# Performance work log

Measured on AMD Instinct MI355X. Metric: run time of the kernel, lower is better.

The kernel has to match this reference:

```python
import jax, jax.numpy as jnp
import numpy as np

B, C, D, H = 128, 8, 1024, 8
K_RANGE = (2, 3, 4, 5)


def setup_inputs() -> dict:
    key = jax.random.key(0)
    ks = jax.random.split(key, 10)
    s = 0.02
    return {
        "x": jax.random.normal(ks[0], (B, D), jnp.float32),
        # per-K prototype groups, shape (nb_classes, K, embed_dim) as in get_prototype_group()
        "p2": jax.random.normal(ks[1], (C, 2, D), jnp.float32),
        "p3": jax.random.normal(ks[2], (C, 3, D), jnp.float32),
        "p4": jax.random.normal(ks[3], (C, 4, D), jnp.float32),
        "p5": jax.random.normal(ks[4], (C, 5, D), jnp.float32),
        # per-class attention Block params (stacked over class axis)
        "ln_g": jnp.ones((C, D), jnp.float32),
        "ln_b": jnp.zeros((C, D), jnp.float32),
        "w_qkv": jax.random.normal(ks[5], (C, 3 * D, D), jnp.float32) * s,
        "b_qkv": jnp.zeros((C, 3 * D), jnp.float32),
        "w_proj": jax.random.normal(ks[6], (C, D, D), jnp.float32) * s,
        "b_proj": jnp.zeros((C, D), jnp.float32),
        # cls head
        "w_cls": jax.random.normal(ks[7], (C, D), jnp.float32) * s,
        "b_cls": jnp.zeros((C,), jnp.float32),
    }


def _proto_group(x, pg):
    """x: (B,D); pg: (C,K,D). Returns nearest proto (B,D), per-sample class group (B,K,D), class ids (B,)."""
    Cc, K, d = pg.shape
    flat = pg.reshape(Cc * K, d)
    # squared L2 distances (argmin identical to torch.cdist p=2 argmin)
    d2 = (jnp.sum(x * x, axis=1, keepdims=True)
          - 2.0 * (x @ flat.T)
          + jnp.sum(flat * flat, axis=1))
    idx = jnp.argmin(d2, axis=1)          # (B,)
    cls = idx // K                        # (B,)
    return flat[idx], pg[cls], cls


def _vicreg(x, nearest, proto_space, sim_c=25.0, std_c=25.0, cov_c=1.0):
    # sim: pull x toward its nearest prototype in every K-group
    repr_loss = jnp.mean((x[:, None, :] - nearest) ** 2)
    # std over batch of prototype space, unbiased var, eps=1e-4
    std = jnp.sqrt(jnp.var(proto_space, axis=0, ddof=1) + 1e-4)   # (S,D)
    std_loss = jnp.mean(jax.nn.relu(1.0 - std))
    # covariance of centered flattened prototype space
    ps = proto_space - jnp.mean(proto_space, axis=0)
    P = ps.reshape(-1, ps.shape[-1])                              # (B*S, D)
    cov = P.T @ P / (P.shape[0] - 1)
    cov_loss = ((cov ** 2).sum() - (jnp.diagonal(cov) ** 2).sum()) / ps.shape[-1]
    return sim_c * repr_loss + std_c * std_loss + cov_c * cov_loss


def _forward(x, p2, p3, p4, p5, ln_g, ln_b, w_qkv, b_qkv, w_proj, b_proj, w_cls, b_cls):
    groups = (p2, p3, p4, p5)
    nearest_list, space_list, cls = [], [], None
    for pg in groups:
        n, sp, cls = _proto_group(x, pg)   # cls kept from LAST group, as in torch code
        nearest_list.append(n)
        space_list.append(sp)
    nearest = jnp.stack(nearest_list, axis=1)     # (B, len(K_range), D)
    proto_space = jnp.concatenate(space_list, 1)  # (B, sum(K_range), D)

    vcr = _vicreg(x, nearest, proto_space)

    # per-class attention Block: LayerNorm -> MHA -> residual, vectorized over class axis c
    S = proto_space.shape[1]
    mu = proto_space.mean(-1, keepdims=True)
    var = proto_space.var(-1, keepdims=True)
    xn = (proto_space - mu) * jax.lax.rsqrt(var + 1e-5)               # (B,S,D)
    h = xn[None] * ln_g[:, None, None, :] + ln_b[:, None, None, :]    # (C,B,S,D)

    qkv = jnp.einsum('cbsd,cfd->cbsf', h, w_qkv) + b_qkv[:, None, None, :]
    dh = D // H
    qkv = qkv.reshape(C, B, S, 3, H, dh).transpose(3, 0, 1, 4, 2, 5)  # (3,C,B,H,S,dh)
    q, k, v = qkv[0] * (dh ** -0.5), qkv[1], qkv[2]
    attn = jax.nn.softmax(jnp.einsum('cbhqe,cbhke->cbhqk', q, k), axis=-1)
    o = jnp.einsum('cbhqk,cbhke->cbhqe', attn, v)                     # (C,B,H,S,dh)
    o = o.transpose(0, 1, 3, 2, 4).reshape(C, B, S, D)
    out = jnp.einsum('cbsd,ced->cbse', o, w_proj) + b_proj[:, None, None, :]
    attended = proto_space[None] + out                                # (C,B,S,D)

    # route each sample through the block of its (last-group) assigned class
    cond = attended[cls, jnp.arange(B)]                               # (B,S,D)
    cond = cond / jnp.maximum(jnp.linalg.norm(cond, axis=2, keepdims=True), 1e-12)
    pooled = cond.mean(1)                                             # (B,D)
    logits = pooled @ w_cls.T + b_cls
    return logits, vcr


def reference(x, p2, p3, p4, p5, ln_g, ln_b, w_qkv, b_qkv, w_proj, b_proj, w_cls, b_cls):
    return _forward(x, p2, p3, p4, p5, ln_g, ln_b, w_qkv, b_qkv, w_proj, b_proj, w_cls, b_cls)
```

## Files before the change

kernel.cpp:

```cpp
#include <hip/hip_runtime.h>
#include <math.h>

#define NB 128
#define ND 1024
#define NS 14
#define NDH 128

typedef float f32x4 __attribute__((ext_vector_type(4)));
typedef short bf16x8 __attribute__((ext_vector_type(8)));
typedef unsigned int u32x4 __attribute__((ext_vector_type(4)));

__device__ __forceinline__ unsigned short f2bf(float v) {
  unsigned int u = __builtin_bit_cast(unsigned int, v);
  return (unsigned short)((u + 0x7FFFu + ((u >> 16) & 1u)) >> 16);
}
__device__ __forceinline__ float bf2f(unsigned short u) {
  return __builtin_bit_cast(float, (unsigned int)u << 16);
}

__device__ __forceinline__ bf16x8 pack_bv(float4 w0, float4 w1) {
  unsigned int u0, u1, u2, u3;
  asm("v_cvt_pk_bf16_f32 %0, %1, %2" : "=v"(u0) : "v"(w0.x), "v"(w0.y));
  asm("v_cvt_pk_bf16_f32 %0, %1, %2" : "=v"(u1) : "v"(w0.z), "v"(w0.w));
  asm("v_cvt_pk_bf16_f32 %0, %1, %2" : "=v"(u2) : "v"(w1.x), "v"(w1.y));
  asm("v_cvt_pk_bf16_f32 %0, %1, %2" : "=v"(u3) : "v"(w1.z), "v"(w1.w));
  u32x4 u = {u0, u1, u2, u3};
  return __builtin_bit_cast(bf16x8, u);
}

__device__ __forceinline__ void s_decomp(int s, int& g, int& k) {
  if (s < 2)      { g = 0; k = s; }
  else if (s < 5) { g = 1; k = s - 2; }
  else if (s < 9) { g = 2; k = s - 5; }
  else            { g = 3; k = s - 9; }
}
__device__ __forceinline__ const float* grp_ptr(int g, const float* p2, const float* p3,
                                                const float* p4, const float* p5) {
  return g == 0 ? p2 : g == 1 ? p3 : g == 2 ? p4 : p5;
}
__device__ __forceinline__ int grp_base(int g) { return g == 0 ? 0 : g == 1 ? 16 : g == 2 ? 40 : 72; }
__device__ __forceinline__ int grp_k(int g) { return g + 2; }

__global__ __launch_bounds__(256) void k_assign_ln(
    const float* __restrict__ x,
    const float* __restrict__ p2, const float* __restrict__ p3,
    const float* __restrict__ p4, const float* __restrict__ p5,
    const float* __restrict__ ln_g, const float* __restrict__ ln_b,
    unsigned short* __restrict__ hbf2, float* __restrict__ pall,
    int* __restrict__ cls, int* __restrict__ rows_g, float* __restrict__ minv)
{
  int bid = blockIdx.x, t = threadIdx.x;
  __shared__ __align__(16) float xs[ND];
  float4* xs4 = (float4*)xs;
  if (bid < 112) {
    int r = bid;
    const float* pp; int idx;
    if (r < 16)      { pp = p2; idx = r; }
    else if (r < 40) { pp = p3; idx = r - 16; }
    else if (r < 72) { pp = p4; idx = r - 40; }
    else             { pp = p5; idx = r - 72; }
    const float4* row4 = (const float4*)(pp + (size_t)idx * ND);
    float4 v = row4[t];
    xs4[t] = v;
    float s1 = v.x + v.y + v.z + v.w;
    float s2 = v.x * v.x + v.y * v.y + v.z * v.z + v.w * v.w;
    __shared__ float ra[256], rb[256];
    ra[t] = s1; rb[t] = s2; __syncthreads();
    for (int o = 128; o > 0; o >>= 1) { if (t < o) { ra[t] += ra[t + o]; rb[t] += rb[t + o]; } __syncthreads(); }
    __shared__ float mu, rstd;
    if (t == 0) {
      float m = ra[0] * (1.f / 1024.f);
      float var = rb[0] * (1.f / 1024.f) - m * m;
      mu = m; rstd = rsqrtf(var + 1e-5f);
    }
    __syncthreads();
    ((float4*)(pall + (size_t)r * ND))[t] = xs4[t];
    float4 xv = xs4[t];
    float nx = (xv.x - mu) * rstd, ny = (xv.y - mu) * rstd,
          nz = (xv.z - mu) * rstd, nw = (xv.w - mu) * rstd;
    int d0 = t * 4;
    int m = r >> 4, rr = r & 15;
    int kblk = d0 >> 5, qq = (d0 >> 3) & 3, e0 = d0 & 7;
    size_t fidx = (size_t)kblk * 3584 + m * 512 + (qq * 16 + rr) * 8 + e0;
#pragma unroll
    for (int c = 0; c < 8; ++c) {
      float4 g = ((const float4*)(ln_g + (size_t)c * ND))[t];
      float4 bb = ((const float4*)(ln_b + (size_t)c * ND))[t];
      ushort4 u;
      u.x = f2bf(nx * g.x + bb.x); u.y = f2bf(ny * g.y + bb.y);
      u.z = f2bf(nz * g.z + bb.z); u.w = f2bf(nw * g.w + bb.w);
      *(ushort4*)&hbf2[(size_t)c * 114688 + fidx] = u;
    }
  } else {
    int b = bid - 112;
    __shared__ float d2s[112];
    __shared__ int cls_s[4];
    const float4* xg4 = (const float4*)(x + (size_t)b * ND);
    xs4[t] = xg4[t];
    __syncthreads();
    if (t < 112) {
      const float* pp; int idx;
      if (t < 16)      { pp = p2; idx = t; }
      else if (t < 40) { pp = p3; idx = t - 16; }
      else if (t < 72) { pp = p4; idx = t - 40; }
      else             { pp = p5; idx = t - 72; }
      const float4* pr4 = (const float4*)(pp + (size_t)idx * ND);
      float acc = 0.f;
#pragma unroll 8
      for (int d = 0; d < 256; ++d) {
        float4 a = xs4[d], p = pr4[d];
        float dx = a.x - p.x, dy = a.y - p.y, dz = a.z - p.z, dw = a.w - p.w;
        acc += dx * dx + dy * dy + dz * dz + dw * dw;
      }
      d2s[t] = acc;
    }
    __syncthreads();
    if (t < 4) {
      int base = grp_base(t), kg = grp_k(t), cnt = 8 * kg;
      float mv = d2s[base]; int mi = 0;
      for (int j = 1; j < cnt; ++j) { float v = d2s[base + j]; if (v < mv) { mv = v; mi = j; } }
      int c = mi / kg;
      cls[b * 4 + t] = c; cls_s[t] = c;
      minv[b * 4 + t] = mv;
    }
    __syncthreads();
    if (t < NS) {
      int g, k; s_decomp(t, g, k);
      rows_g[b * NS + t] = grp_base(g) + cls_s[g] * grp_k(g) + k;
    }
  }
}

__global__ __launch_bounds__(128) void k_prep(
    const int* __restrict__ cls, const float* __restrict__ minv,
    int* __restrict__ counts, int* __restrict__ ccnt, int* __restrict__ order,
    int* __restrict__ posof, int* __restrict__ chunkidx, int* __restrict__ chunk_c,
    int* __restrict__ chunk_lo, int* __restrict__ chunkN, float* __restrict__ scal)
{
  __shared__ int cnt_s[32];
  __shared__ int cc_s[8];
  __shared__ float red[128];
  int t = threadIdx.x;
  if (t < 32) cnt_s[t] = 0;
  if (t < 8) cc_s[t] = 0;
  if (t < 4) scal[t] = 0.f;
  __syncthreads();
  int c3;
#pragma unroll
  for (int g = 0; g < 4; ++g) {
    int c = cls[t * 4 + g];
    atomicAdd(&cnt_s[g * 8 + c], 1);
    if (g == 3) c3 = c;
  }
  int pos = atomicAdd(&cc_s[c3], 1);
  order[c3 * 128 + pos] = t;
  posof[t] = pos;
  red[t] = minv[t * 4 + 0] + minv[t * 4 + 1] + minv[t * 4 + 2] + minv[t * 4 + 3];
  __syncthreads();
  for (int o = 64; o > 0; o >>= 1) { if (t < o) red[t] += red[t + o]; __syncthreads(); }
  if (t == 0) {
    scal[0] = red[0];
    int T = 0;
    for (int c = 0; c < 8; ++c) {
      chunkidx[c] = T;
      int nch = (cc_s[c] + 15) >> 4;
      for (int j = 0; j < nch; ++j) { chunk_c[T] = c; chunk_lo[T] = j * 16; ++T; }
    }
    chunkN[0] = T;
  }
  if (t < 32) counts[t] = cnt_s[t];
  if (t < 8) ccnt[t] = cc_s[t];
}

__global__ __launch_bounds__(256) void k_stats(
    const float* __restrict__ p2, const float* __restrict__ p3,
    const float* __restrict__ p4, const float* __restrict__ p5,
    const int* __restrict__ counts, float* __restrict__ M, float* __restrict__ scal)
{
  int idx = blockIdx.x * 256 + threadIdx.x;
  int s = idx >> 10, d = idx & 1023;
  int g, k; s_decomp(s, g, k);
  const float* pp = grp_ptr(g, p2, p3, p4, p5);
  int kg = grp_k(g);
  float vc[8], nc[8];
  float sum = 0.f, sumsq = 0.f;
#pragma unroll
  for (int c = 0; c < 8; ++c) {
    float v = pp[((size_t)(c * kg + k)) * ND + d];
    float n = (float)counts[g * 8 + c];
    vc[c] = v; nc[c] = n;
    sum += n * v; sumsq += n * v * v;
  }
  float mean = sum * (1.f / 128.f);
  float var = (sumsq - 128.f * mean * mean) * (1.f / 127.f);
  float sd = sqrtf(var + 1e-4f);
#pragma unroll
  for (int c = 0; c < 8; ++c)
    M[((size_t)(s * 8 + c)) * ND + d] = sqrtf(nc[c] * (1.f / 1791.f)) * (vc[c] - mean);
  float part = fmaxf(1.f - sd, 0.f);
  __shared__ float red[256];
  red[threadIdx.x] = part; __syncthreads();
  for (int o = 128; o > 0; o >>= 1) { if (threadIdx.x < o) red[threadIdx.x] += red[threadIdx.x + o]; __syncthreads(); }
  if (threadIdx.x == 0) atomicAdd(&scal[1], red[0]);
}

__global__ __launch_bounds__(128) void k_gramdiag(const float* __restrict__ M, float* __restrict__ scal)
{
  __shared__ __align__(16) float mi[ND];
  __shared__ float red[128];
  int bid = blockIdx.x, t = threadIdx.x;
  if (bid < 112) {
    float4* mi4 = (float4*)mi;
    const float4* src4 = (const float4*)(M + (size_t)bid * ND);
    for (int d = t; d < 256; d += 128) mi4[d] = src4[d];
    __syncthreads();
    float p = 0.f;
    if (t < 112) {
      const float4* mj4 = (const float4*)(M + (size_t)t * ND);
      float acc = 0.f;
#pragma unroll 8
      for (int d = 0; d < 256; ++d) {
        float4 a = mi4[d], b = mj4[d];
        acc += a.x * b.x + a.y * b.y + a.z * b.z + a.w * b.w;
      }
      p = acc * acc;
    }
    red[t] = p; __syncthreads();
    for (int o = 64; o > 0; o >>= 1) { if (t < o) red[t] += red[t + o]; __syncthreads(); }
    if (t == 0) atomicAdd(&scal[2], red[0]);
  } else {
    int d = (bid - 112) * 128 + t;
    float tsum = 0.f;
    for (int r = 0; r < 112; ++r) { float v = M[(size_t)r * ND + d]; tsum += v * v; }
    red[t] = tsum * tsum; __syncthreads();
    for (int o = 64; o > 0; o >>= 1) { if (t < o) red[t] += red[t + o]; __syncthreads(); }
    if (t == 0) atomicAdd(&scal[3], red[0]);
  }
}

__global__ __launch_bounds__(512) void k_qkv_mfma(
    const unsigned short* __restrict__ hbf2, const float* __restrict__ w_qkv,
    const float* __restrict__ b_qkv, unsigned short* __restrict__ qkv_bf)
{
  __shared__ __align__(16) float lred[3 * 2 * 7 * 256];
  int c = blockIdx.y;
  int t = threadIdx.x, lane = t & 63, wid = t >> 6;
  int cg = wid & 1, ks = wid >> 1;
  int r16 = lane & 15, q = lane >> 4;
  int col = blockIdx.x * 32 + cg * 16 + r16;
  const float* Wp = w_qkv + ((size_t)c * 3072 + col) * ND + ks * 256 + q * 8;
  const unsigned short* Hp = hbf2 + (size_t)c * 114688 + (size_t)(ks * 8) * 3584 + lane * 8;
  f32x4 acc[7] = {};
#pragma unroll
  for (int i = 0; i < 8; ++i) {
    float4 w0 = *(const float4*)(Wp + i * 32);
    float4 w1 = *(const float4*)(Wp + i * 32 + 4);
    bf16x8 bv = pack_bv(w0, w1);
    const unsigned short* hk = Hp + (size_t)i * 3584;
#pragma unroll
    for (int m = 0; m < 7; ++m) {
      bf16x8 av = *(const bf16x8*)(hk + m * 512);
      acc[m] = __builtin_amdgcn_mfma_f32_16x16x32_bf16(av, bv, acc[m], 0, 0, 0);
    }
  }
  if (ks) {
#pragma unroll
    for (int m = 0; m < 7; ++m)
      *(f32x4*)&lred[(((ks - 1) * 2 + cg) * 7 + m) * 256 + lane * 4] = acc[m];
  }
  __syncthreads();
  if (ks == 0) {
    float bq = b_qkv[(size_t)c * 3072 + col];
#pragma unroll
    for (int m = 0; m < 7; ++m) {
      f32x4 a1 = *(const f32x4*)&lred[((0 * 2 + cg) * 7 + m) * 256 + lane * 4];
      f32x4 a2 = *(const f32x4*)&lred[((1 * 2 + cg) * 7 + m) * 256 + lane * 4];
      f32x4 a3 = *(const f32x4*)&lred[((2 * 2 + cg) * 7 + m) * 256 + lane * 4];
#pragma unroll
      for (int r = 0; r < 4; ++r) {
        int row = m * 16 + q * 4 + r;
        qkv_bf[((size_t)c * 112 + row) * 3072 + col] = f2bf(acc[m][r] + a1[r] + a2[r] + a3[r] + bq);
      }
    }
  }
}

__global__ __launch_bounds__(256) void k_attn(
    const unsigned short* __restrict__ qkv_bf, const int* __restrict__ cls,
    const int* __restrict__ rows_g, const int* __restrict__ posof,
    const int* __restrict__ chunkidx, unsigned short* __restrict__ obf2)
{
  __shared__ __align__(16) float qs[NS * NDH], ks2[NS * NDH], vs[NS * NDH];
  __shared__ float sc[NS * NS];
  __shared__ int rg[NS];
  int h = blockIdx.x, b = blockIdx.y, t = threadIdx.x;
  if (t < NS) rg[t] = rows_g[b * NS + t];
  __syncthreads();
  int cp = cls[b * 4 + 3];
  int pos = posof[b];
  size_t gbase = (size_t)(chunkidx[cp] + (pos >> 4)) * 229376;
  int slot = pos & 15;
  const float scale = 0.08838834764831843f;
  for (int i = t; i < NS * 64; i += 256) {
    int s = i >> 6, e2 = (i & 63) * 2;
    size_t base = ((size_t)cp * 112 + rg[s]) * 3072 + h * NDH + e2;
    unsigned int uq = *(const unsigned int*)&qkv_bf[base];
    unsigned int uk = *(const unsigned int*)&qkv_bf[base + 1024];
    unsigned int uv = *(const unsigned int*)&qkv_bf[base + 2048];
    qs[s * NDH + e2]      = bf2f((unsigned short)uq) * scale;
    qs[s * NDH + e2 + 1]  = bf2f((unsigned short)(uq >> 16)) * scale;
    ks2[s * NDH + e2]     = bf2f((unsigned short)uk);
    ks2[s * NDH + e2 + 1] = bf2f((unsigned short)(uk >> 16));
    vs[s * NDH + e2]      = bf2f((unsigned short)uv);
    vs[s * NDH + e2 + 1]  = bf2f((unsigned short)(uv >> 16));
  }
  __syncthreads();
  if (t < NS * NS) {
    int si = t / NS, sj = t - (t / NS) * NS;
    const float4* qa = (const float4*)&qs[si * NDH];
    const float4* kb = (const float4*)&ks2[sj * NDH];
    float acc = 0.f;
#pragma unroll 8
    for (int e4 = 0; e4 < 32; ++e4) {
      float4 a = qa[e4], k4 = kb[e4];
      acc += a.x * k4.x + a.y * k4.y + a.z * k4.z + a.w * k4.w;
    }
    sc[t] = acc;
  }
  __syncthreads();
  if (t < NS) {
    float mx = -1e30f;
    for (int j = 0; j < NS; ++j) mx = fmaxf(mx, sc[t * NS + j]);
    float e_[NS]; float sum = 0.f;
    for (int j = 0; j < NS; ++j) { float e = expf(sc[t * NS + j] - mx); e_[j] = e; sum += e; }
    float inv = 1.f / sum;
    for (int j = 0; j < NS; ++j) sc[t * NS + j] = e_[j] * inv;
  }
  __syncthreads();
  for (int i = t; i < NS * 32; i += 256) {
    int s = i >> 5, e4 = i & 31;
    float4 a = {0.f, 0.f, 0.f, 0.f};
#pragma unroll
    for (int j = 0; j < NS; ++j) {
      float w = sc[s * NS + j];
      float4 v4 = ((const float4*)&vs[j * NDH])[e4];
      a.x += w * v4.x; a.y += w * v4.y; a.z += w * v4.z; a.w += w * v4.w;
    }
    int row = slot * 14 + s;
    int m = row >> 4, r16 = row & 15;
    int d0 = h * NDH + e4 * 4;
    int kblk = d0 >> 5, qq = (d0 >> 3) & 3, e0 = d0 & 7;
    ushort4 u; u.x = f2bf(a.x); u.y = f2bf(a.y); u.z = f2bf(a.z); u.w = f2bf(a.w);
    *(ushort4*)&obf2[gbase + (size_t)kblk * 7168 + m * 512 + (qq * 16 + r16) * 8 + e0] = u;
  }
}

__global__ __launch_bounds__(512) void k_proj_mfma(
    const unsigned short* __restrict__ obf2, const int* __restrict__ order,
    const int* __restrict__ ccnt, const int* __restrict__ chunk_c,
    const int* __restrict__ chunk_lo, const int* __restrict__ chunkN,
    const int* __restrict__ rows_g,
    const float* __restrict__ w_proj, const float* __restrict__ b_proj,
    const float* __restrict__ pall, float* __restrict__ att)
{
  int g = blockIdx.y;
  if (g >= chunkN[0]) return;
  __shared__ __align__(16) float lred[3 * 2 * 7 * 256];
  __shared__ int sid_s[16];
  int c = chunk_c[g], lo = chunk_lo[g];
  int cnt = ccnt[c];
  int nb = cnt - lo; if (nb > 16) nb = 16;
  int t = threadIdx.x, lane = t & 63, wid = t >> 6;
  int rh = wid & 1, ks = wid >> 1;
  if (t < 16) sid_s[t] = order[c * 128 + lo + ((t < nb) ? t : nb - 1)];
  int r16 = lane & 15, q = lane >> 4;
  int col = blockIdx.x * 16 + r16;
  const float* Wp = w_proj + ((size_t)c * ND + col) * ND + ks * 256 + q * 8;
  const unsigned short* Ap = obf2 + (size_t)g * 229376 + (size_t)(ks * 8) * 7168 + rh * 3584 + lane * 8;
  f32x4 acc[7] = {};
#pragma unroll
  for (int i = 0; i < 8; ++i) {
    float4 w0 = *(const float4*)(Wp + i * 32);
    float4 w1 = *(const float4*)(Wp + i * 32 + 4);
    bf16x8 bv = pack_bv(w0, w1);
    const unsigned short* ak = Ap + (size_t)i * 7168;
#pragma unroll
    for (int m = 0; m < 7; ++m) {
      bf16x8 av = *(const bf16x8*)(ak + m * 512);
      acc[m] = __builtin_amdgcn_mfma_f32_16x16x32_bf16(av, bv, acc[m], 0, 0, 0);
    }
  }
  if (ks) {
#pragma unroll
    for (int m = 0; m < 7; ++m)
      *(f32x4*)&lred[(((ks - 1) * 2 + rh) * 7 + m) * 256 + lane * 4] = acc[m];
  }
  __syncthreads();
  if (ks == 0) {
    float bp = b_proj[(size_t)c * ND + col];
#pragma unroll
    for (int m = 0; m < 7; ++m) {
      f32x4 a1 = *(const f32x4*)&lred[((0 * 2 + rh) * 7 + m) * 256 + lane * 4];
      f32x4 a2 = *(const f32x4*)&lred[((1 * 2 + rh) * 7 + m) * 256 + lane * 4];
      f32x4 a3 = *(const f32x4*)&lred[((2 * 2 + rh) * 7 + m) * 256 + lane * 4];
#pragma unroll
      for (int r = 0; r < 4; ++r) {
        int row = rh * 112 + m * 16 + q * 4 + r;
        int slot = row / 14, s = row - slot * 14;
        if (slot < nb) {
          int b = sid_s[slot];
          float res = pall[(size_t)rows_g[b * NS + s] * ND + col];
          att[((size_t)b * NS + s) * ND + col] = acc[m][r] + a1[r] + a2[r] + a3[r] + bp + res;
        }
      }
    }
  }
}

__global__ __launch_bounds__(256) void k_final(
    const float* __restrict__ att, const float* __restrict__ w_cls,
    const float* __restrict__ b_cls, const float* __restrict__ scal,
    float* __restrict__ out)
{
  int b = blockIdx.x, t = threadIdx.x;
  __shared__ __align__(16) float as[NS * ND];
  __shared__ float wred[NS][4];
  __shared__ float inv[NS];
  __shared__ __align__(16) float pooled[ND];
  int lane = t & 63, w = t >> 6;
#pragma unroll
  for (int s = 0; s < NS; ++s) {
    float4 v = ((const float4*)(att + ((size_t)b * NS + s) * ND))[t];
    ((float4*)&as[s * ND])[t] = v;
    float p = v.x * v.x + v.y * v.y + v.z * v.z + v.w * v.w;
#pragma unroll
    for (int o = 32; o > 0; o >>= 1) p += __shfl_xor(p, o, 64);
    if (lane == 0) wred[s][w] = p;
  }
  __syncthreads();
  if (t < NS) {
    float s2 = wred[t][0] + wred[t][1] + wred[t][2] + wred[t][3];
    inv[t] = 1.f / fmaxf(sqrtf(s2), 1e-12f);
  }
  __syncthreads();
  float4 pa = {0.f, 0.f, 0.f, 0.f};
#pragma unroll
  for (int s = 0; s < NS; ++s) {
    float iv = inv[s];
    float4 v = ((const float4*)&as[s * ND])[t];
    pa.x += iv * v.x; pa.y += iv * v.y; pa.z += iv * v.z; pa.w += iv * v.w;
  }
  const float k14 = 1.f / 14.f;
  pa.x *= k14; pa.y *= k14; pa.z *= k14; pa.w *= k14;
  ((float4*)pooled)[t] = pa;
  __syncthreads();
  int c = t >> 5, l = t & 31;
  float acc = 0.f;
#pragma unroll
  for (int k = 0; k < 8; ++k) {
    int i4 = l + k * 32;
    float4 p4 = ((const float4*)pooled)[i4];
    float4 wc = ((const float4*)(w_cls + (size_t)c * ND))[i4];
    acc += p4.x * wc.x + p4.y * wc.y + p4.z * wc.z + p4.w * wc.w;
  }
  for (int o = 16; o > 0; o >>= 1) acc += __shfl_down(acc, o, 32);
  if (l == 0) out[b * 8 + c] = acc + b_cls[c];
  if (b == 0 && t == 0) {
    float repr = scal[0] * (1.f / (128.f * 4.f * 1024.f));
    float stdl = scal[1] * (1.f / 14336.f);
    float covl = (scal[2] - scal[3]) * (1.f / 1024.f);
    out[1024] = 25.f * repr + 25.f * stdl + covl;
  }
}

extern "C" void kernel_launch(void* const* d_in, const int* in_sizes, int n_in,
                              void* d_out, int out_size, void* d_ws, size_t ws_size,
                              hipStream_t stream) {
  const float* x      = (const float*)d_in[0];
  const float* p2     = (const float*)d_in[1];
  const float* p3     = (const float*)d_in[2];
  const float* p4     = (const float*)d_in[3];
  const float* p5     = (const float*)d_in[4];
  const float* ln_g   = (const float*)d_in[5];
  const float* ln_b   = (const float*)d_in[6];
  const float* w_qkv  = (const float*)d_in[7];
  const float* b_qkv  = (const float*)d_in[8];
  const float* w_proj = (const float*)d_in[9];
  const float* b_proj = (const float*)d_in[10];
  const float* w_cls  = (const float*)d_in[11];
  const float* b_cls  = (const float*)d_in[12];
  float* out = (float*)d_out;
  char* ws = (char*)d_ws;

  float* scal      = (float*)(ws + 0);
  int*   counts    = (int*)(ws + 64);
  int*   ccnt      = (int*)(ws + 192);
  int*   cls       = (int*)(ws + 256);
  int*   rows_g    = (int*)(ws + 2304);
  int*   order     = (int*)(ws + 9472);
  float* minv      = (float*)(ws + 13568);
  int*   posof     = (int*)(ws + 15616);
  int*   chunkidx  = (int*)(ws + 16128);
  int*   chunk_c   = (int*)(ws + 16160);
  int*   chunk_lo  = (int*)(ws + 16224);
  int*   chunkN    = (int*)(ws + 16288);
  float* pall      = (float*)(ws + 16384);
  unsigned short* hbf2 = (unsigned short*)(ws + 475136);
  unsigned short* qkvb = (unsigned short*)(ws + 2310144);
  unsigned short* obf2 = (unsigned short*)(ws + 7815168);
  float* att       = (float*)(ws + 15155200);
  float* M         = (float*)(ws + 22495232);

  k_assign_ln<<<240, 256, 0, stream>>>(x, p2, p3, p4, p5, ln_g, ln_b, hbf2, pall, cls, rows_g, minv);
  k_qkv_mfma<<<dim3(96, 8), 512, 0, stream>>>(hbf2, w_qkv, b_qkv, qkvb);
  k_prep<<<1, 128, 0, stream>>>(cls, minv, counts, ccnt, order, posof, chunkidx, chunk_c, chunk_lo, chunkN, scal);
  k_stats<<<56, 256, 0, stream>>>(p2, p3, p4, p5, counts, M, scal);
  k_gramdiag<<<120, 128, 0, stream>>>(M, scal);
  k_attn<<<dim3(8, 128), 256, 0, stream>>>(qkvb, cls, rows_g, posof, chunkidx, obf2);
  k_proj_mfma<<<dim3(64, 15), 512, 0, stream>>>(obf2, order, ccnt, chunk_c, chunk_lo, chunkN, rows_g, w_proj, b_proj, pall, att);
  k_final<<<128, 256, 0, stream>>>(att, w_cls, b_cls, scal, out);
}
```

Baseline: 141.0 us.

## Merge independent stages into shared launches to cut kernel count and idle time

Regroups eight launches into six by pairing independent work in the same grid. The prototype assignment now runs in the QKV GEMM launch, the VICReg std stats run in the attention launch, and the covariance gram and diagonal run in the projection GEMM launch. The gram kernel is also reworked to split each dot product over four threads, and the attention loader reads four bf16 values at a time. This cuts launch gaps and lets small serial kernels overlap with large ones, at the cost of mixed-role blocks that share LDS budgets and launch bounds.

```diff
diff --git a/kernel.cpp b/kernel.cpp
--- a/kernel.cpp
+++ b/kernel.cpp
@@ -41,62 +41,114 @@
 __device__ __forceinline__ int grp_base(int g) { return g == 0 ? 0 : g == 1 ? 16 : g == 2 ? 40 : 72; }
 __device__ __forceinline__ int grp_k(int g) { return g + 2; }
 
-__global__ __launch_bounds__(256) void k_assign_ln(
+__global__ __launch_bounds__(256) void k_ln(
+    const float* __restrict__ p2, const float* __restrict__ p3,
+    const float* __restrict__ p4, const float* __restrict__ p5,
+    const float* __restrict__ ln_g, const float* __restrict__ ln_b,
+    unsigned short* __restrict__ hbf2, float* __restrict__ pall)
+{
+  int r = blockIdx.x, t = threadIdx.x;
+  __shared__ __align__(16) float xs[ND];
+  float4* xs4 = (float4*)xs;
+  const float* pp; int idx;
+  if (r < 16)      { pp = p2; idx = r; }
+  else if (r < 40) { pp = p3; idx = r - 16; }
+  else if (r < 72) { pp = p4; idx = r - 40; }
+  else             { pp = p5; idx = r - 72; }
+  const float4* row4 = (const float4*)(pp + (size_t)idx * ND);
+  float4 v = row4[t];
+  xs4[t] = v;
+  float s1 = v.x + v.y + v.z + v.w;
+  float s2 = v.x * v.x + v.y * v.y + v.z * v.z + v.w * v.w;
+  __shared__ float ra[256], rb[256];
+  ra[t] = s1; rb[t] = s2; __syncthreads();
+  for (int o = 128; o > 0; o >>= 1) { if (t < o) { ra[t] += ra[t + o]; rb[t] += rb[t + o]; } __syncthreads(); }
+  __shared__ float mu, rstd;
+  if (t == 0) {
+    float m = ra[0] * (1.f / 1024.f);
+    float var = rb[0] * (1.f / 1024.f) - m * m;
+    mu = m; rstd = rsqrtf(var + 1e-5f);
+  }
+  __syncthreads();
+  ((float4*)(pall + (size_t)r * ND))[t] = xs4[t];
+  float4 xv = xs4[t];
+  float nx = (xv.x - mu) * rstd, ny = (xv.y - mu) * rstd,
+        nz = (xv.z - mu) * rstd, nw = (xv.w - mu) * rstd;
+  int d0 = t * 4;
+  int m = r >> 4, rr = r & 15;
+  int kblk = d0 >> 5, qq = (d0 >> 3) & 3, e0 = d0 & 7;
+  size_t fidx = (size_t)kblk * 3584 + m * 512 + (qq * 16 + rr) * 8 + e0;
+#pragma unroll
+  for (int c = 0; c < 8; ++c) {
+    float4 g = ((const float4*)(ln_g + (size_t)c * ND))[t];
+    float4 bb = ((const float4*)(ln_b + (size_t)c * ND))[t];
+    ushort4 u;
+    u.x = f2bf(nx * g.x + bb.x); u.y = f2bf(ny * g.y + bb.y);
+    u.z = f2bf(nz * g.z + bb.z); u.w = f2bf(nw * g.w + bb.w);
+    *(ushort4*)&hbf2[(size_t)c * 114688 + fidx] = u;
+  }
+}
+
+__global__ __launch_bounds__(512) void k_qkv_assign(
+    const unsigned short* __restrict__ hbf2, const float* __restrict__ w_qkv,
+    const float* __restrict__ b_qkv, unsigned short* __restrict__ qkv_bf,
     const float* __restrict__ x,
     const float* __restrict__ p2, const float* __restrict__ p3,
     const float* __restrict__ p4, const float* __restrict__ p5,
-    const float* __restrict__ ln_g, const float* __restrict__ ln_b,
-    unsigned short* __restrict__ hbf2, float* __restrict__ pall,
     int* __restrict__ cls, int* __restrict__ rows_g, float* __restrict__ minv)
 {
+  __shared__ __align__(16) float lred[3 * 2 * 7 * 256];
   int bid = blockIdx.x, t = threadIdx.x;
-  __shared__ __align__(16) float xs[ND];
-  float4* xs4 = (float4*)xs;
-  if (bid < 112) {
-    int r = bid;
-    const float* pp; int idx;
-    if (r < 16)      { pp = p2; idx = r; }
-    else if (r < 40) { pp = p3; idx = r - 16; }
-    else if (r < 72) { pp = p4; idx = r - 40; }
-    else             { pp = p5; idx = r - 72; }
-    const float4* row4 = (const float4*)(pp + (size_t)idx * ND);
-    float4 v = row4[t];
-    xs4[t] = v;
-    float s1 = v.x + v.y + v.z + v.w;
-    float s2 = v.x * v.x + v.y * v.y + v.z * v.z + v.w * v.w;
-    __shared__ float ra[256], rb[256];
-    ra[t] = s1; rb[t] = s2; __syncthreads();
-    for (int o = 128; o > 0; o >>= 1) { if (t < o) { ra[t] += ra[t + o]; rb[t] += rb[t + o]; } __syncthreads(); }
-    __shared__ float mu, rstd;
-    if (t == 0) {
-      float m = ra[0] * (1.f / 1024.f);
-      float var = rb[0] * (1.f / 1024.f) - m * m;
-      mu = m; rstd = rsqrtf(var + 1e-5f);
-    }
-    __syncthreads();
-    ((float4*)(pall + (size_t)r * ND))[t] = xs4[t];
-    float4 xv = xs4[t];
-    float nx = (xv.x - mu) * rstd, ny = (xv.y - mu) * rstd,
-          nz = (xv.z - mu) * rstd, nw = (xv.w - mu) * rstd;
-    int d0 = t * 4;
-    int m = r >> 4, rr = r & 15;
-    int kblk = d0 >> 5, qq = (d0 >> 3) & 3, e0 = d0 & 7;
-    size_t fidx = (size_t)kblk * 3584 + m * 512 + (qq * 16 + rr) * 8 + e0;
-#pragma unroll
-    for (int c = 0; c < 8; ++c) {
-      float4 g = ((const float4*)(ln_g + (size_t)c * ND))[t];
-      float4 bb = ((const float4*)(ln_b + (size_t)c * ND))[t];
-      ushort4 u;
-      u.x = f2bf(nx * g.x + bb.x); u.y = f2bf(ny * g.y + bb.y);
-      u.z = f2bf(nz * g.z + bb.z); u.w = f2bf(nw * g.w + bb.w);
-      *(ushort4*)&hbf2[(size_t)c * 114688 + fidx] = u;
+  if (bid < 768) {
+    int c = bid / 96, xb = bid - c * 96;
+    int lane = t & 63, wid = t >> 6;
+    int cg = wid & 1, ks = wid >> 1;
+    int r16 = lane & 15, q = lane >> 4;
+    int col = xb * 32 + cg * 16 + r16;
+    const float* Wp = w_qkv + ((size_t)c * 3072 + col) * ND + ks * 256 + q * 8;
+    const unsigned short* Hp = hbf2 + (size_t)c * 114688 + (size_t)(ks * 8) * 3584 + lane * 8;
+    f32x4 acc[7] = {};
+#pragma unroll
+    for (int i = 0; i < 8; ++i) {
+      float4 w0 = *(const float4*)(Wp + i * 32);
+      float4 w1 = *(const float4*)(Wp + i * 32 + 4);
+      bf16x8 bv = pack_bv(w0, w1);
+      const unsigned short* hk = Hp + (size_t)i * 3584;
+#pragma unroll
+      for (int m = 0; m < 7; ++m) {
+        bf16x8 av = *(const bf16x8*)(hk + m * 512);
+        acc[m] = __builtin_amdgcn_mfma_f32_16x16x32_bf16(av, bv, acc[m], 0, 0, 0);
+      }
+    }
+    if (ks) {
+#pragma unroll
+      for (int m = 0; m < 7; ++m)
+        *(f32x4*)&lred[(((ks - 1) * 2 + cg) * 7 + m) * 256 + lane * 4] = acc[m];
+    }
+    __syncthreads();
+    if (ks == 0) {
+      float bq = b_qkv[(size_t)c * 3072 + col];
+#pragma unroll
+      for (int m = 0; m < 7; ++m) {
+        f32x4 a1 = *(const f32x4*)&lred[((0 * 2 + cg) * 7 + m) * 256 + lane * 4];
+        f32x4 a2 = *(const f32x4*)&lred[((1 * 2 + cg) * 7 + m) * 256 + lane * 4];
+        f32x4 a3 = *(const f32x4*)&lred[((2 * 2 + cg) * 7 + m) * 256 + lane * 4];
+#pragma unroll
+        for (int r = 0; r < 4; ++r) {
+          int row = m * 16 + q * 4 + r;
+          qkv_bf[((size_t)c * 112 + row) * 3072 + col] = f2bf(acc[m][r] + a1[r] + a2[r] + a3[r] + bq);
+        }
+      }
     }
   } else {
-    int b = bid - 112;
-    __shared__ float d2s[112];
-    __shared__ int cls_s[4];
-    const float4* xg4 = (const float4*)(x + (size_t)b * ND);
-    xs4[t] = xg4[t];
+    int b = bid - 768;
+    float4* xs4 = (float4*)lred;
+    float* d2s = lred + 1024;
+    int* cls_s = (int*)(lred + 1152);
+    if (t < 256) {
+      const float4* xg4 = (const float4*)(x + (size_t)b * ND);
+      xs4[t] = xg4[t];
+    }
     __syncthreads();
     if (t < 112) {
       const float* pp; int idx;
@@ -172,248 +224,207 @@
   if (t < 8) ccnt[t] = cc_s[t];
 }
 
-__global__ __launch_bounds__(256) void k_stats(
+__global__ __launch_bounds__(256) void k_attn_stats(
+    const unsigned short* __restrict__ qkv_bf, const int* __restrict__ cls,
+    const int* __restrict__ rows_g, const int* __restrict__ posof,
+    const int* __restrict__ chunkidx, unsigned short* __restrict__ obf2,
     const float* __restrict__ p2, const float* __restrict__ p3,
     const float* __restrict__ p4, const float* __restrict__ p5,
     const int* __restrict__ counts, float* __restrict__ M, float* __restrict__ scal)
 {
-  int idx = blockIdx.x * 256 + threadIdx.x;
-  int s = idx >> 10, d = idx & 1023;
-  int g, k; s_decomp(s, g, k);
-  const float* pp = grp_ptr(g, p2, p3, p4, p5);
-  int kg = grp_k(g);
-  float vc[8], nc[8];
-  float sum = 0.f, sumsq = 0.f;
-#pragma unroll
-  for (int c = 0; c < 8; ++c) {
-    float v = pp[((size_t)(c * kg + k)) * ND + d];
-    float n = (float)counts[g * 8 + c];
-    vc[c] = v; nc[c] = n;
-    sum += n * v; sumsq += n * v * v;
-  }
-  float mean = sum * (1.f / 128.f);
-  float var = (sumsq - 128.f * mean * mean) * (1.f / 127.f);
-  float sd = sqrtf(var + 1e-4f);
-#pragma unroll
-  for (int c = 0; c < 8; ++c)
-    M[((size_t)(s * 8 + c)) * ND + d] = sqrtf(nc[c] * (1.f / 1791.f)) * (vc[c] - mean);
-  float part = fmaxf(1.f - sd, 0.f);
-  __shared__ float red[256];
-  red[threadIdx.x] = part; __syncthreads();
-  for (int o = 128; o > 0; o >>= 1) { if (threadIdx.x < o) red[threadIdx.x] += red[threadIdx.x + o]; __syncthreads(); }
-  if (threadIdx.x == 0) atomicAdd(&scal[1], red[0]);
-}
-
-__global__ __launch_bounds__(128) void k_gramdiag(const float* __restrict__ M, float* __restrict__ scal)
-{
-  __shared__ __align__(16) float mi[ND];
-  __shared__ float red[128];
   int bid = blockIdx.x, t = threadIdx.x;
-  if (bid < 112) {
-    float4* mi4 = (float4*)mi;
-    const float4* src4 = (const float4*)(M + (size_t)bid * ND);
-    for (int d = t; d < 256; d += 128) mi4[d] = src4[d];
-    __syncthreads();
-    float p = 0.f;
-    if (t < 112) {
-      const float4* mj4 = (const float4*)(M + (size_t)t * ND);
+  if (bid < 1024) {
+    __shared__ __align__(16) float qs[NS * NDH], ks2[NS * NDH], vs[NS * NDH];
+    __shared__ float sc[NS * NS];
+    __shared__ int rg[NS];
+    int h = bid & 7, b = bid >> 3;
+    if (t < NS) rg[t] = rows_g[b * NS + t];
+    __syncthreads();
+    int cp = cls[b * 4 + 3];
+    int pos = posof[b];
+    size_t gbase = (size_t)(chunkidx[cp] + (pos >> 4)) * 229376;
+    int slot = pos & 15;
+    const float scale = 0.08838834764831843f;
+    for (int i = t; i < NS * 32; i += 256) {
+      int s = i >> 5, e4 = (i & 31) * 4;
+      size_t base = ((size_t)cp * 112 + rg[s]) * 3072 + h * NDH + e4;
+      ushort4 uq = *(const ushort4*)&qkv_bf[base];
+      ushort4 uk = *(const ushort4*)&qkv_bf[base + 1024];
+      ushort4 uv = *(const ushort4*)&qkv_bf[base + 2048];
+      int o = s * NDH + e4;
+      qs[o]     = bf2f(uq.x) * scale; qs[o + 1] = bf2f(uq.y) * scale;
+      qs[o + 2] = bf2f(uq.z) * scale; qs[o + 3] = bf2f(uq.w) * scale;
+      ks2[o]     = bf2f(uk.x); ks2[o + 1] = bf2f(uk.y);
+      ks2[o + 2] = bf2f(uk.z); ks2[o + 3] = bf2f(uk.w);
+      vs[o]     = bf2f(uv.x); vs[o + 1] = bf2f(uv.y);
+      vs[o + 2] = bf2f(uv.z); vs[o + 3] = bf2f(uv.w);
+    }
+    __syncthreads();
+    if (t < NS * NS) {
+      int si = t / NS, sj = t - (t / NS) * NS;
+      const float4* qa = (const float4*)&qs[si * NDH];
+      const float4* kb = (const float4*)&ks2[sj * NDH];
       float acc = 0.f;
 #pragma unroll 8
-      for (int d = 0; d < 256; ++d) {
-        float4 a = mi4[d], b = mj4[d];
-        acc += a.x * b.x + a.y * b.y + a.z * b.z + a.w * b.w;
-      }
-      p = acc * acc;
-    }
-    red[t] = p; __syncthreads();
-    for (int o = 64; o > 0; o >>= 1) { if (t < o) red[t] += red[t + o]; __syncthreads(); }
-    if (t == 0) atomicAdd(&scal[2], red[0]);
+      for (int e4 = 0; e4 < 32; ++e4) {
+        float4 a = qa[e4], k4 = kb[e4];
+        acc += a.x * k4.x + a.y * k4.y + a.z * k4.z + a.w * k4.w;
+      }
+      sc[t] = acc;
+    }
+    __syncthreads();
+    if (t < NS) {
+      float mx = -1e30f;
+      for (int j = 0; j < NS; ++j) mx = fmaxf(mx, sc[t * NS + j]);
+      float e_[NS]; float sum = 0.f;
+      for (int j = 0; j < NS; ++j) { float e = expf(sc[t * NS + j] - mx); e_[j] = e; sum += e; }
+      float inv = 1.f / sum;
+      for (int j = 0; j < NS; ++j) sc[t * NS + j] = e_[j] * inv;
+    }
+    __syncthreads();
+    for (int i = t; i < NS * 32; i += 256) {
+      int s = i >> 5, e4 = i & 31;
+      float4 a = {0.f, 0.f, 0.f, 0.f};
+#pragma unroll
+      for (int j = 0; j < NS; ++j) {
+        float w = sc[s * NS + j];
+        float4 v4 = ((const float4*)&vs[j * NDH])[e4];
+        a.x += w * v4.x; a.y += w * v4.y; a.z += w * v4.z; a.w += w * v4.w;
+      }
+      int row = slot * 14 + s;
+      int m = row >> 4, r16 = row & 15;
+      int d0 = h * NDH + e4 * 4;
+      int kblk = d0 >> 5, qq = (d0 >> 3) & 3, e0 = d0 & 7;
+      ushort4 u; u.x = f2bf(a.x); u.y = f2bf(a.y); u.z = f2bf(a.z); u.w = f2bf(a.w);
+      *(ushort4*)&obf2[gbase + (size_t)kblk * 7168 + m * 512 + (qq * 16 + r16) * 8 + e0] = u;
+    }
   } else {
-    int d = (bid - 112) * 128 + t;
-    float tsum = 0.f;
-    for (int r = 0; r < 112; ++r) { float v = M[(size_t)r * ND + d]; tsum += v * v; }
-    red[t] = tsum * tsum; __syncthreads();
-    for (int o = 64; o > 0; o >>= 1) { if (t < o) red[t] += red[t + o]; __syncthreads(); }
-    if (t == 0) atomicAdd(&scal[3], red[0]);
-  }
-}
-
-__global__ __launch_bounds__(512) void k_qkv_mfma(
-    const unsigned short* __restrict__ hbf2, const float* __restrict__ w_qkv,
-    const float* __restrict__ b_qkv, unsigned short* __restrict__ qkv_bf)
-{
-  __shared__ __align__(16) float lred[3 * 2 * 7 * 256];
-  int c = blockIdx.y;
-  int t = threadIdx.x, lane = t & 63, wid = t >> 6;
-  int cg = wid & 1, ks = wid >> 1;
-  int r16 = lane & 15, q = lane >> 4;
-  int col = blockIdx.x * 32 + cg * 16 + r16;
-  const float* Wp = w_qkv + ((size_t)c * 3072 + col) * ND + ks * 256 + q * 8;
-  const unsigned short* Hp = hbf2 + (size_t)c * 114688 + (size_t)(ks * 8) * 3584 + lane * 8;
-  f32x4 acc[7] = {};
-#pragma unroll
-  for (int i = 0; i < 8; ++i) {
-    float4 w0 = *(const float4*)(Wp + i * 32);
-    float4 w1 = *(const float4*)(Wp + i * 32 + 4);
-    bf16x8 bv = pack_bv(w0, w1);
-    const unsigned short* hk = Hp + (size_t)i * 3584;
-#pragma unroll
-    for (int m = 0; m < 7; ++m) {
-      bf16x8 av = *(const bf16x8*)(hk + m * 512);
-      acc[m] = __builtin_amdgcn_mfma_f32_16x16x32_bf16(av, bv, acc[m], 0, 0, 0);
-    }
-  }
-  if (ks) {
-#pragma unroll
-    for (int m = 0; m < 7; ++m)
-      *(f32x4*)&lred[(((ks - 1) * 2 + cg) * 7 + m) * 256 + lane * 4] = acc[m];
-  }
-  __syncthreads();
-  if (ks == 0) {
-    float bq = b_qkv[(size_t)c * 3072 + col];
-#pragma unroll
-    for (int m = 0; m < 7; ++m) {
-      f32x4 a1 = *(const f32x4*)&lred[((0 * 2 + cg) * 7 + m) * 256 + lane * 4];
-      f32x4 a2 = *(const f32x4*)&lred[((1 * 2 + cg) * 7 + m) * 256 + lane * 4];
-      f32x4 a3 = *(const f32x4*)&lred[((2 * 2 + cg) * 7 + m) * 256 + lane * 4];
-#pragma unroll
-      for (int r = 0; r < 4; ++r) {
-        int row = m * 16 + q * 4 + r;
-        qkv_bf[((size_t)c * 112 + row) * 3072 + col] = f2bf(acc[m][r] + a1[r] + a2[r] + a3[r] + bq);
-      }
-    }
-  }
-}
-
-__global__ __launch_bounds__(256) void k_attn(
-    const unsigned short* __restrict__ qkv_bf, const int* __restrict__ cls,
-    const int* __restrict__ rows_g, const int* __restrict__ posof,
-    const int* __restrict__ chunkidx, unsigned short* __restrict__ obf2)
-{
-  __shared__ __align__(16) float qs[NS * NDH], ks2[NS * NDH], vs[NS * NDH];
-  __shared__ float sc[NS * NS];
-  __shared__ int rg[NS];
-  int h = blockIdx.x, b = blockIdx.y, t = threadIdx.x;
-  if (t < NS) rg[t] = rows_g[b * NS + t];
-  __syncthreads();
-  int cp = cls[b * 4 + 3];
-  int pos = posof[b];
-  size_t gbase = (size_t)(chunkidx[cp] + (pos >> 4)) * 229376;
-  int slot = pos & 15;
-  const float scale = 0.08838834764831843f;
-  for (int i = t; i < NS * 64; i += 256) {
-    int s = i >> 6, e2 = (i & 63) * 2;
-    size_t base = ((size_t)cp * 112 + rg[s]) * 3072 + h * NDH + e2;
-    unsigned int uq = *(const unsigned int*)&qkv_bf[base];
-    unsigned int uk = *(const unsigned int*)&qkv_bf[base + 1024];
-    unsigned int uv = *(const unsigned int*)&qkv_bf[base + 2048];
-    qs[s * NDH + e2]      = bf2f((unsigned short)uq) * scale;
-    qs[s * NDH + e2 + 1]  = bf2f((unsigned short)(uq >> 16)) * scale;
-    ks2[s * NDH + e2]     = bf2f((unsigned short)uk);
-    ks2[s * NDH + e2 + 1] = bf2f((unsigned short)(uk >> 16));
-    vs[s * NDH + e2]      = bf2f((unsigned short)uv);
-    vs[s * NDH + e2 + 1]  = bf2f((unsigned short)(uv >> 16));
-  }
-  __syncthreads();
-  if (t < NS * NS) {
-    int si = t / NS, sj = t - (t / NS) * NS;
-    const float4* qa = (const float4*)&qs[si * NDH];
-    const float4* kb = (const float4*)&ks2[sj * NDH];
-    float acc = 0.f;
-#pragma unroll 8
-    for (int e4 = 0; e4 < 32; ++e4) {
-      float4 a = qa[e4], k4 = kb[e4];
-      acc += a.x * k4.x + a.y * k4.y + a.z * k4.z + a.w * k4.w;
-    }
-    sc[t] = acc;
-  }
-  __syncthreads();
-  if (t < NS) {
-    float mx = -1e30f;
-    for (int j = 0; j < NS; ++j) mx = fmaxf(mx, sc[t * NS + j]);
-    float e_[NS]; float sum = 0.f;
-    for (int j = 0; j < NS; ++j) { float e = expf(sc[t * NS + j] - mx); e_[j] = e; sum += e; }
-    float inv = 1.f / sum;
-    for (int j = 0; j < NS; ++j) sc[t * NS + j] = e_[j] * inv;
-  }
-  __syncthreads();
-  for (int i = t; i < NS * 32; i += 256) {
-    int s = i >> 5, e4 = i & 31;
-    float4 a = {0.f, 0.f, 0.f, 0.f};
-#pragma unroll
-    for (int j = 0; j < NS; ++j) {
-      float w = sc[s * NS + j];
-      float4 v4 = ((const float4*)&vs[j * NDH])[e4];
-      a.x += w * v4.x; a.y += w * v4.y; a.z += w * v4.z; a.w += w * v4.w;
-    }
-    int row = slot * 14 + s;
-    int m = row >> 4, r16 = row & 15;
-    int d0 = h * NDH + e4 * 4;
-    int kblk = d0 >> 5, qq = (d0 >> 3) & 3, e0 = d0 & 7;
-    ushort4 u; u.x = f2bf(a.x); u.y = f2bf(a.y); u.z = f2bf(a.z); u.w = f2bf(a.w);
-    *(ushort4*)&obf2[gbase + (size_t)kblk * 7168 + m * 512 + (qq * 16 + r16) * 8 + e0] = u;
-  }
-}
-
-__global__ __launch_bounds__(512) void k_proj_mfma(
+    int idx = (bid - 1024) * 256 + t;
+    int s = idx >> 10, d = idx & 1023;
+    int g, k; s_decomp(s, g, k);
+    const float* pp = grp_ptr(g, p2, p3, p4, p5);
+    int kg = grp_k(g);
+    float vc[8], nc[8];
+    float sum = 0.f, sumsq = 0.f;
+#pragma unroll
+    for (int c = 0; c < 8; ++c) {
+      float v = pp[((size_t)(c * kg + k)) * ND + d];
+      float n = (float)counts[g * 8 + c];
+      vc[c] = v; nc[c] = n;
+      sum += n * v; sumsq += n * v * v;
+    }
+    float mean = sum * (1.f / 128.f);
+    float var = (sumsq - 128.f * mean * mean) * (1.f / 127.f);
+    float sd = sqrtf(var + 1e-4f);
+#pragma unroll
+    for (int c = 0; c < 8; ++c)
+      M[((size_t)(s * 8 + c)) * ND + d] = sqrtf(nc[c] * (1.f / 1791.f)) * (vc[c] - mean);
+    float part = fmaxf(1.f - sd, 0.f);
+    __shared__ float red[256];
+    red[t] = part; __syncthreads();
+    for (int o = 128; o > 0; o >>= 1) { if (t < o) red[t] += red[t + o]; __syncthreads(); }
+    if (t == 0) atomicAdd(&scal[1], red[0]);
+  }
+}
+
+__global__ __launch_bounds__(512) void k_proj_gram(
     const unsigned short* __restrict__ obf2, const int* __restrict__ order,
     const int* __restrict__ ccnt, const int* __restrict__ chunk_c,
     const int* __restrict__ chunk_lo, const int* __restrict__ chunkN,
     const int* __restrict__ rows_g,
     const float* __restrict__ w_proj, const float* __restrict__ b_proj,
-    const float* __restrict__ pall, float* __restrict__ att)
+    const float* __restrict__ pall, float* __restrict__ att,
+    const float* __restrict__ M, float* __restrict__ scal)
 {
-  int g = blockIdx.y;
-  if (g >= chunkN[0]) return;
-  __shared__ __align__(16) float lred[3 * 2 * 7 * 256];
-  __shared__ int sid_s[16];
-  int c = chunk_c[g], lo = chunk_lo[g];
-  int cnt = ccnt[c];
-  int nb = cnt - lo; if (nb > 16) nb = 16;
-  int t = threadIdx.x, lane = t & 63, wid = t >> 6;
-  int rh = wid & 1, ks = wid >> 1;
-  if (t < 16) sid_s[t] = order[c * 128 + lo + ((t < nb) ? t : nb - 1)];
-  int r16 = lane & 15, q = lane >> 4;
-  int col = blockIdx.x * 16 + r16;
-  const float* Wp = w_proj + ((size_t)c * ND + col) * ND + ks * 256 + q * 8;
-  const unsigned short* Ap = obf2 + (size_t)g * 229376 + (size_t)(ks * 8) * 7168 + rh * 3584 + lane * 8;
-  f32x4 acc[7] = {};
-#pragma unroll
-  for (int i = 0; i < 8; ++i) {
-    float4 w0 = *(const float4*)(Wp + i * 32);
-    float4 w1 = *(const float4*)(Wp + i * 32 + 4);
-    bf16x8 bv = pack_bv(w0, w1);
-    const unsigned short* ak = Ap + (size_t)i * 7168;
-#pragma unroll
-    for (int m = 0; m < 7; ++m) {
-      bf16x8 av = *(const bf16x8*)(ak + m * 512);
-      acc[m] = __builtin_amdgcn_mfma_f32_16x16x32_bf16(av, bv, acc[m], 0, 0, 0);
-    }
-  }
-  if (ks) {
-#pragma unroll
-    for (int m = 0; m < 7; ++m)
-      *(f32x4*)&lred[(((ks - 1) * 2 + rh) * 7 + m) * 256 + lane * 4] = acc[m];
-  }
-  __syncthreads();
-  if (ks == 0) {
-    float bp = b_proj[(size_t)c * ND + col];
-#pragma unroll
-    for (int m = 0; m < 7; ++m) {
-      f32x4 a1 = *(const f32x4*)&lred[((0 * 2 + rh) * 7 + m) * 256 + lane * 4];
-      f32x4 a2 = *(const f32x4*)&lred[((1 * 2 + rh) * 7 + m) * 256 + lane * 4];
-      f32x4 a3 = *(const f32x4*)&lred[((2 * 2 + rh) * 7 + m) * 256 + lane * 4];
-#pragma unroll
-      for (int r = 0; r < 4; ++r) {
-        int row = rh * 112 + m * 16 + q * 4 + r;
-        int slot = row / 14, s = row - slot * 14;
-        if (slot < nb) {
-          int b = sid_s[slot];
-          float res = pall[(size_t)rows_g[b * NS + s] * ND + col];
-          att[((size_t)b * NS + s) * ND + col] = acc[m][r] + a1[r] + a2[r] + a3[r] + bp + res;
+  int bid = blockIdx.x, t = threadIdx.x;
+  if (bid < 960) {
+    int g = bid / 64, xb = bid - g * 64;
+    if (g >= chunkN[0]) return;
+    __shared__ __align__(16) float lred[3 * 2 * 7 * 256];
+    __shared__ int sid_s[16];
+    int c = chunk_c[g], lo = chunk_lo[g];
+    int cnt = ccnt[c];
+    int nb = cnt - lo; if (nb > 16) nb = 16;
+    int lane = t & 63, wid = t >> 6;
+    int rh = wid & 1, ks = wid >> 1;
+    if (t < 16) sid_s[t] = order[c * 128 + lo + ((t < nb) ? t : nb - 1)];
+    int r16 = lane & 15, q = lane >> 4;
+    int col = xb * 16 + r16;
+    const float* Wp = w_proj + ((size_t)c * ND + col) * ND + ks * 256 + q * 8;
+    const unsigned short* Ap = obf2 + (size_t)g * 229376 + (size_t)(ks * 8) * 7168 + rh * 3584 + lane * 8;
+    f32x4 acc[7] = {};
+#pragma unroll
+    for (int i = 0; i < 8; ++i) {
+      float4 w0 = *(const float4*)(Wp + i * 32);
+      float4 w1 = *(const float4*)(Wp + i * 32 + 4);
+      bf16x8 bv = pack_bv(w0, w1);
+      const unsigned short* ak = Ap + (size_t)i * 7168;
+#pragma unroll
+      for (int m = 0; m < 7; ++m) {
+        bf16x8 av = *(const bf16x8*)(ak + m * 512);
+        acc[m] = __builtin_amdgcn_mfma_f32_16x16x32_bf16(av, bv, acc[m], 0, 0, 0);
+      }
+    }
+    if (ks) {
+#pragma unroll
+      for (int m = 0; m < 7; ++m)
+        *(f32x4*)&lred[(((ks - 1) * 2 + rh) * 7 + m) * 256 + lane * 4] = acc[m];
+    }
+    __syncthreads();
+    if (ks == 0) {
+      float bp = b_proj[(size_t)c * ND + col];
+#pragma unroll
+      for (int m = 0; m < 7; ++m) {
+        f32x4 a1 = *(const f32x4*)&lred[((0 * 2 + rh) * 7 + m) * 256 + lane * 4];
+        f32x4 a2 = *(const f32x4*)&lred[((1 * 2 + rh) * 7 + m) * 256 + lane * 4];
+        f32x4 a3 = *(const f32x4*)&lred[((2 * 2 + rh) * 7 + m) * 256 + lane * 4];
+#pragma unroll
+        for (int r = 0; r < 4; ++r) {
+          int row = rh * 112 + m * 16 + q * 4 + r;
+          int slot = row / 14, s = row - slot * 14;
+          if (slot < nb) {
+            int b = sid_s[slot];
+            float res = pall[(size_t)rows_g[b * NS + s] * ND + col];
+            att[((size_t)b * NS + s) * ND + col] = acc[m][r] + a1[r] + a2[r] + a3[r] + bp + res;
+          }
         }
       }
     }
+  } else if (bid < 1072) {
+    int r = bid - 960;
+    __shared__ __align__(16) float mi[ND];
+    __shared__ float red2[128];
+    float4* mi4 = (float4*)mi;
+    const float4* src4 = (const float4*)(M + (size_t)r * ND);
+    if (t < 256) mi4[t] = src4[t];
+    if (t < 128) red2[t] = 0.f;
+    __syncthreads();
+    int j = t >> 2, qd = t & 3;
+    float p = 0.f;
+    if (j < 112) {
+      const float4* mj4 = (const float4*)(M + (size_t)j * ND);
+      float acc = 0.f;
+#pragma unroll 8
+      for (int d = qd * 64; d < qd * 64 + 64; ++d) {
+        float4 a = mi4[d], b = mj4[d];
+        acc += a.x * b.x + a.y * b.y + a.z * b.z + a.w * b.w;
+      }
+      acc += __shfl_xor(acc, 1, 4);
+      acc += __shfl_xor(acc, 2, 4);
+      p = acc * acc;
+    }
+    if (qd == 0 && j < 112) red2[j] = p;
+    __syncthreads();
+    for (int o = 64; o > 0; o >>= 1) { if (t < o) red2[t] += red2[t + o]; __syncthreads(); }
+    if (t == 0) atomicAdd(&scal[2], red2[0]);
+  } else {
+    int d = (bid - 1072) * 512 + t;
+    float tsum = 0.f;
+    for (int r = 0; r < 112; ++r) { float v = M[(size_t)r * ND + d]; tsum += v * v; }
+    __shared__ float red3[512];
+    red3[t] = tsum * tsum; __syncthreads();
+    for (int o = 256; o > 0; o >>= 1) { if (t < o) red3[t] += red3[t + o]; __syncthreads(); }
+    if (t == 0) atomicAdd(&scal[3], red3[0]);
   }
 }
 
@@ -511,12 +522,13 @@
   float* att       = (float*)(ws + 15155200);
   float* M         = (float*)(ws + 22495232);
 
-  k_assign_ln<<<240, 256, 0, stream>>>(x, p2, p3, p4, p5, ln_g, ln_b, hbf2, pall, cls, rows_g, minv);
-  k_qkv_mfma<<<dim3(96, 8), 512, 0, stream>>>(hbf2, w_qkv, b_qkv, qkvb);
+  k_ln<<<112, 256, 0, stream>>>(p2, p3, p4, p5, ln_g, ln_b, hbf2, pall);
+  k_qkv_assign<<<896, 512, 0, stream>>>(hbf2, w_qkv, b_qkv, qkvb,
+                                        x, p2, p3, p4, p5, cls, rows_g, minv);
   k_prep<<<1, 128, 0, stream>>>(cls, minv, counts, ccnt, order, posof, chunkidx, chunk_c, chunk_lo, chunkN, scal);
-  k_stats<<<56, 256, 0, stream>>>(p2, p3, p4, p5, counts, M, scal);
-  k_gramdiag<<<120, 128, 0, stream>>>(M, scal);
-  k_attn<<<dim3(8, 128), 256, 0, stream>>>(qkvb, cls, rows_g, posof, chunkidx, obf2);
-  k_proj_mfma<<<dim3(64, 15), 512, 0, stream>>>(obf2, order, ccnt, chunk_c, chunk_lo, chunkN, rows_g, w_proj, b_proj, pall, att);
+  k_attn_stats<<<1080, 256, 0, stream>>>(qkvb, cls, rows_g, posof, chunkidx, obf2,
+                                         p2, p3, p4, p5, counts, M, scal);
+  k_proj_gram<<<1074, 512, 0, stream>>>(obf2, order, ccnt, chunk_c, chunk_lo, chunkN, rows_g,
+                                        w_proj, b_proj, pall, att, M, scal);
   k_final<<<128, 256, 0, stream>>>(att, w_cls, b_cls, scal, out);
 }
```

Result: faster. 124.0 us (-12.1%).
